# Optimization experiments

Measured on AMD Instinct MI355X. Metric: run time of the kernel, lower is better.

The kernel has to match this reference:

```python
import jax, jax.numpy as jnp
import numpy as np

B = 256      # events
N_SV = 64    # secondary vertices per event
N_TRK = 512  # tracks per event
N_PFC = 512  # PF candidates per event
K = 8        # kNN neighbors
H = 32       # hidden dim


def _lin_init(key, fan_in, fan_out):
    k1, k2 = jax.random.split(key)
    lim = 1.0 / np.sqrt(fan_in)
    W = jax.random.uniform(k1, (fan_in, fan_out), minval=-lim, maxval=lim, dtype=jnp.float32)
    b = jax.random.uniform(k2, (fan_out,), minval=-lim, maxval=lim, dtype=jnp.float32)
    return W, b


def setup_inputs() -> dict:
    key = jax.random.key(0)
    ks = jax.random.split(key, 16)
    inp = {
        'x_sv': jax.random.normal(ks[0], (B * N_SV, 14), dtype=jnp.float32),
        'x_trk': jax.random.normal(ks[1], (B * N_TRK, 30), dtype=jnp.float32),
        'x_pfc': jax.random.normal(ks[2], (B * N_PFC, 10), dtype=jnp.float32),
        'batch_sv': jnp.repeat(jnp.arange(B, dtype=jnp.int64), N_SV),
        'batch_trk': jnp.repeat(jnp.arange(B, dtype=jnp.int64), N_TRK),
        'batch_pfc': jnp.repeat(jnp.arange(B, dtype=jnp.int64), N_PFC),
    }
    inp['sv_W1'], inp['sv_b1'] = _lin_init(ks[3], 14, H)
    inp['sv_W2'], inp['sv_b2'] = _lin_init(ks[4], H, H)
    inp['trk_W1'], inp['trk_b1'] = _lin_init(ks[5], 30, H)
    inp['trk_W2'], inp['trk_b2'] = _lin_init(ks[6], H, H)
    inp['pfc_W1'], inp['pfc_b1'] = _lin_init(ks[7], 10, H)
    inp['pfc_W2'], inp['pfc_b2'] = _lin_init(ks[8], H, H)
    inp['conv_W'], inp['conv_b'] = _lin_init(ks[9], 2 * H, H)  # the single shared self.conv
    inp['out_W1'], inp['out_b1'] = _lin_init(ks[10], H, H)
    inp['out_W2'], inp['out_b2'] = _lin_init(ks[11], H, 1)
    return inp


def _encode(x, W1, b1, W2, b2):
    h = jax.nn.elu(x @ W1 + b1)
    return jax.nn.elu(h @ W2 + b2)


def _edge_conv(x_src, x_dst, W, b):
    # x_src [B,Ns,H] source set, x_dst [B,Nd,H] destination/query set.
    # kNN: for each dst node, K nearest src nodes (per event) by Euclidean dist.
    d2 = (jnp.sum(x_dst * x_dst, -1)[:, :, None]
          - 2.0 * jnp.einsum('bnd,bmd->bnm', x_dst, x_src)
          + jnp.sum(x_src * x_src, -1)[:, None, :])  # [B,Nd,Ns]
    _, idx = jax.lax.top_k(-d2, K)                     # [B,Nd,K]
    x_j = jax.vmap(lambda s, i: s[i])(x_src, idx)      # [B,Nd,K,H]
    x_i = jnp.broadcast_to(x_dst[:, :, None, :], x_j.shape)
    e = jnp.concatenate([x_i, x_j - x_i], axis=-1)     # [B,Nd,K,2H]
    m = jax.nn.elu(e @ W + b)                          # edge MLP
    return jnp.max(m, axis=2)                          # max aggregation [B,Nd,H]


def reference(x_sv, x_trk, x_pfc, batch_sv, batch_trk, batch_pfc,
              sv_W1, sv_b1, sv_W2, sv_b2,
              trk_W1, trk_b1, trk_W2, trk_b2,
              pfc_W1, pfc_b1, pfc_W2, pfc_b2,
              conv_W, conv_b, out_W1, out_b1, out_W2, out_b2):
    sv = _encode(x_sv, sv_W1, sv_b1, sv_W2, sv_b2).reshape(B, N_SV, H)
    trk = _encode(x_trk, trk_W1, trk_b1, trk_W2, trk_b2).reshape(B, N_TRK, H)
    pfc = _encode(x_pfc, pfc_W1, pfc_b1, pfc_W2, pfc_b2).reshape(B, N_PFC, H)

    feats1 = _edge_conv(sv, trk, conv_W, conv_b)     # sv -> trk
    feats2 = _edge_conv(pfc, trk, conv_W, conv_b)    # pfc -> trk
    feats3 = _edge_conv(feats1, feats2, conv_W, conv_b)  # feats1 -> feats2 (both trk-sized)

    # avg_pool_x(batch_trk, feats3, batch_trk): per-event mean
    f = feats3.reshape(B * N_TRK, H)
    s = jax.ops.segment_sum(f, batch_trk, num_segments=B)
    cnt = jax.ops.segment_sum(jnp.ones((B * N_TRK,), f.dtype), batch_trk, num_segments=B)
    pooled = s / cnt[:, None]

    out = jax.nn.sigmoid(jax.nn.elu(pooled @ out_W1 + out_b1) @ out_W2 + out_b2)  # [B,1]
    return out, jnp.arange(B, dtype=jnp.int64)
```

## Files before the change

### kernel.cpp

```cpp
#include <hip/hip_runtime.h>
#include <math.h>

#define NB 256
#define KNN 8

typedef __attribute__((ext_vector_type(8))) short short8;
typedef __attribute__((ext_vector_type(4))) float f32x4;

__device__ __forceinline__ float elu_f(float x) {
    return x > 0.f ? x : __expf(x) - 1.f;
}

__device__ __forceinline__ unsigned bf16rn(float x) {
    unsigned u = __float_as_uint(x);
    return (u + 0x7FFFu + ((u >> 16) & 1u)) >> 16;
}

__device__ __forceinline__ void bfsplit(float x, short& h, short& l) {
    unsigned hu = bf16rn(x);
    h = (short)hu;
    l = (short)bf16rn(x - __uint_as_float(hu << 16));
}

__device__ __forceinline__ void cex(unsigned& a, unsigned& b) {
    unsigned lo = min(a, b), hi = max(a, b);
    a = lo; b = hi;
}

__device__ __forceinline__ void sort8(unsigned* s) {
    cex(s[0], s[1]); cex(s[2], s[3]); cex(s[4], s[5]); cex(s[6], s[7]);
    cex(s[0], s[2]); cex(s[1], s[3]); cex(s[4], s[6]); cex(s[5], s[7]);
    cex(s[1], s[2]); cex(s[5], s[6]);
    cex(s[0], s[4]); cex(s[1], s[5]); cex(s[2], s[6]); cex(s[3], s[7]);
    cex(s[2], s[4]); cex(s[3], s[5]);
    cex(s[1], s[2]); cex(s[3], s[4]); cex(s[5], s[6]);
}

__device__ __forceinline__ void merge8(unsigned* v, const unsigned* s) {
#pragma unroll
    for (int i = 0; i < 8; i++) v[i] = min(v[i], s[7 - i]);
    cex(v[0], v[4]); cex(v[1], v[5]); cex(v[2], v[6]); cex(v[3], v[7]);
    cex(v[0], v[2]); cex(v[1], v[3]); cex(v[4], v[6]); cex(v[5], v[7]);
    cex(v[0], v[1]); cex(v[2], v[3]); cex(v[4], v[5]); cex(v[6], v[7]);
}

template<int FIN, int MODE>
__device__ void encode_mfma_body(const float* __restrict__ x,
    const float* __restrict__ W1, const float* __restrict__ b1,
    const float* __restrict__ W2, const float* __restrict__ b2,
    const float* __restrict__ conv_W, const float* __restrict__ conv_b,
    float* __restrict__ enc, float* __restrict__ e1,
    unsigned short* __restrict__ hiP, unsigned short* __restrict__ loP,
    float* __restrict__ nrmP,
    int blk, float* __restrict__ sx)
{
    int tid = threadIdx.x;
    int lane = tid & 63, wv = tid >> 6;
    int c = lane & 15, kg = lane >> 4;
    size_t node0 = (size_t)blk * 256;

    {
        const float* xb = x + node0 * FIN;
        for (int i = tid; i < 8192; i += 256) {
            int n = i >> 5, f = i & 31;
            sx[i] = (f < FIN) ? xb[n * FIN + f] : 0.f;
        }
    }
    __syncthreads();

    int rb = wv * 64;

#pragma unroll
    for (int ph = 0; ph < 3; ph++) {
        short8 Bh0, Bl0, Bh1, Bl1;
#pragma unroll
        for (int e = 0; e < 8; e++) {
            int kk = kg * 8 + e;
            float w0, w1;
            if (ph == 0) {
                w0 = (kk < FIN) ? W1[kk * 32 + c] : 0.f;
                w1 = (kk < FIN) ? W1[kk * 32 + 16 + c] : 0.f;
            } else if (ph == 1) {
                w0 = W2[kk * 32 + c];
                w1 = W2[kk * 32 + 16 + c];
            } else {
                w0 = conv_W[1024 + kk * 32 + c];
                w1 = conv_W[1024 + kk * 32 + 16 + c];
                if (MODE == 1) {
                    w0 = conv_W[kk * 32 + c] - w0;
                    w1 = conv_W[kk * 32 + 16 + c] - w1;
                }
            }
            short h, l;
            bfsplit(w0, h, l); Bh0[e] = h; Bl0[e] = l;
            bfsplit(w1, h, l); Bh1[e] = h; Bl1[e] = l;
        }
        float bias0, bias1;
        if (ph == 0)      { bias0 = b1[c]; bias1 = b1[16 + c]; }
        else if (ph == 1) { bias0 = b2[c]; bias1 = b2[16 + c]; }
        else              { bias0 = (MODE == 1) ? conv_b[c] : 0.f;
                            bias1 = (MODE == 1) ? conv_b[16 + c] : 0.f; }

#pragma unroll
        for (int t = 0; t < 4; t++) {
            int tb = rb + t * 16;
            int arow = tb + c;
            const float* ap = sx + arow * 32 + kg * 8;
            float4 a0 = *(const float4*)(ap);
            float4 a1 = *(const float4*)(ap + 4);
            float av[8] = {a0.x, a0.y, a0.z, a0.w, a1.x, a1.y, a1.z, a1.w};
            short8 Ah, Al;
#pragma unroll
            for (int e = 0; e < 8; e++) {
                short h, l;
                bfsplit(av[e], h, l);
                Ah[e] = h; Al[e] = l;
            }

            if (MODE == 0 && ph == 2) {
                float nr = 0.f;
#pragma unroll
                for (int e = 0; e < 8; e++) nr = fmaf(av[e], av[e], nr);
                nr += __shfl_xor(nr, 16);
                nr += __shfl_xor(nr, 32);
                if (kg == 0) nrmP[node0 + arow] = nr;
                *(short8*)(hiP + (node0 + arow) * 32 + kg * 8) = Ah;
                *(short8*)(loP + (node0 + arow) * 32 + kg * 8) = Al;
            }

            f32x4 acc0 = {bias0, bias0, bias0, bias0};
            f32x4 acc1 = {bias1, bias1, bias1, bias1};
            acc0 = __builtin_amdgcn_mfma_f32_16x16x32_bf16(Al, Bh0, acc0, 0, 0, 0);
            acc0 = __builtin_amdgcn_mfma_f32_16x16x32_bf16(Ah, Bl0, acc0, 0, 0, 0);
            acc0 = __builtin_amdgcn_mfma_f32_16x16x32_bf16(Ah, Bh0, acc0, 0, 0, 0);
            acc1 = __builtin_amdgcn_mfma_f32_16x16x32_bf16(Al, Bh1, acc1, 0, 0, 0);
            acc1 = __builtin_amdgcn_mfma_f32_16x16x32_bf16(Ah, Bl1, acc1, 0, 0, 0);
            acc1 = __builtin_amdgcn_mfma_f32_16x16x32_bf16(Ah, Bh1, acc1, 0, 0, 0);

            int drow = tb + kg * 4;
            if (ph < 2) {
#pragma unroll
                for (int r = 0; r < 4; r++) {
                    float v0 = elu_f(acc0[r]);
                    float v1 = elu_f(acc1[r]);
                    sx[(drow + r) * 32 + c] = v0;
                    sx[(drow + r) * 32 + 16 + c] = v1;
                    if (MODE == 1 && ph == 1) {
                        size_t off = (node0 + drow + r) * 32 + c;
                        enc[off] = v0;
                        enc[off + 16] = v1;
                    }
                }
            } else {
#pragma unroll
                for (int r = 0; r < 4; r++) {
                    size_t off = (node0 + drow + r) * 32 + c;
                    e1[off] = acc0[r];
                    e1[off + 16] = acc1[r];
                }
            }
        }
    }
}

__global__ __launch_bounds__(256) void encode_all_kernel(
    const float* __restrict__ x_sv, const float* __restrict__ x_trk, const float* __restrict__ x_pfc,
    const float* __restrict__ sv_W1, const float* __restrict__ sv_b1,
    const float* __restrict__ sv_W2, const float* __restrict__ sv_b2,
    const float* __restrict__ trk_W1, const float* __restrict__ trk_b1,
    const float* __restrict__ trk_W2, const float* __restrict__ trk_b2,
    const float* __restrict__ pfc_W1, const float* __restrict__ pfc_b1,
    const float* __restrict__ pfc_W2, const float* __restrict__ pfc_b2,
    const float* __restrict__ conv_W, const float* __restrict__ conv_b,
    float* __restrict__ trk_enc,
    float* __restrict__ Y1, float* __restrict__ Y2,
    float* __restrict__ f1base,
    unsigned short* __restrict__ svHi, unsigned short* __restrict__ svLo, float* __restrict__ nrm_sv,
    unsigned short* __restrict__ pfcHi, unsigned short* __restrict__ pfcLo, float* __restrict__ nrm_pfc)
{
    __shared__ float sx[8192];
    int bid = blockIdx.x;
    if (bid < 64)
        encode_mfma_body<14, 0>(x_sv, sv_W1, sv_b1, sv_W2, sv_b2, conv_W, conv_b,
                                nullptr, Y1, svHi, svLo, nrm_sv, bid, sx);
    else if (bid < 576)
        encode_mfma_body<30, 1>(x_trk, trk_W1, trk_b1, trk_W2, trk_b2, conv_W, conv_b,
                                trk_enc, f1base, nullptr, nullptr, nullptr, bid - 64, sx);
    else
        encode_mfma_body<10, 0>(x_pfc, pfc_W1, pfc_b1, pfc_W2, pfc_b2, conv_W, conv_b,
                                nullptr, Y2, pfcHi, pfcLo, nrm_pfc, bid - 576, sx);
}

__device__ __forceinline__ void knn_build_B(const float* __restrict__ dstF,
                                            int dstbase, int c, int kg,
                                            short8& Bh, short8& Bl, float& nd)
{
    const float* brow = dstF + (size_t)(dstbase + c) * 32 + kg * 8;
    float4 b0 = *(const float4*)(brow);
    float4 b1 = *(const float4*)(brow + 4);
    float bx[8] = {b0.x, b0.y, b0.z, b0.w, b1.x, b1.y, b1.z, b1.w};
    nd = 0.f;
#pragma unroll
    for (int i = 0; i < 8; i++) {
        float xv = bx[i];
        nd = fmaf(xv, xv, nd);
        short h, l;
        bfsplit(xv, h, l);
        Bh[i] = h; Bl[i] = l;
    }
    nd += __shfl_xor(nd, 16);
    nd += __shfl_xor(nd, 32);
}

template<int NT>
__device__ __forceinline__ void knn_scan(
    const unsigned short* __restrict__ srcHi, const unsigned short* __restrict__ srcLo,
    const float* __restrict__ snrm,
    short8 Bh, short8 Bl, float nd, int c, int kg,
    unsigned* key)
{
    for (int t = 0; t < NT; t += 2) {
        unsigned cand[8];
#pragma unroll
        for (int u = 0; u < 2; u++) {
            int tt = t + u;
            size_t arow = ((size_t)(tt * 16 + c)) * 32 + (size_t)kg * 8;
            short8 Ah = *(const short8*)(srcHi + arow);
            short8 Al = *(const short8*)(srcLo + arow);
            f32x4 acc = {0.f, 0.f, 0.f, 0.f};
            acc = __builtin_amdgcn_mfma_f32_16x16x32_bf16(Al, Bl, acc, 0, 0, 0);
            acc = __builtin_amdgcn_mfma_f32_16x16x32_bf16(Al, Bh, acc, 0, 0, 0);
            acc = __builtin_amdgcn_mfma_f32_16x16x32_bf16(Ah, Bl, acc, 0, 0, 0);
            acc = __builtin_amdgcn_mfma_f32_16x16x32_bf16(Ah, Bh, acc, 0, 0, 0);
            float4 sn = *(const float4*)(snrm + tt * 16 + kg * 4);
            int sb = tt * 16 + kg * 4;
            cand[u*4+0] = (__float_as_uint(fmaf(-2.f, acc[0], sn.x + nd)) & 0xFFFFFE00u) | (unsigned)(sb + 0);
            cand[u*4+1] = (__float_as_uint(fmaf(-2.f, acc[1], sn.y + nd)) & 0xFFFFFE00u) | (unsigned)(sb + 1);
            cand[u*4+2] = (__float_as_uint(fmaf(-2.f, acc[2], sn.z + nd)) & 0xFFFFFE00u) | (unsigned)(sb + 2);
            cand[u*4+3] = (__float_as_uint(fmaf(-2.f, acc[3], sn.w + nd)) & 0xFFFFFE00u) | (unsigned)(sb + 3);
        }
        sort8(cand);
        merge8(key, cand);
    }
}

__device__ __forceinline__ void knn_merge_lanes(unsigned* key)
{
    unsigned oth[8];
#pragma unroll
    for (int k = 0; k < 8; k++) oth[k] = __shfl_xor(key[k], 16);
    merge8(key, oth);
#pragma unroll
    for (int k = 0; k < 8; k++) oth[k] = __shfl_xor(key[k], 32);
    merge8(key, oth);
}

__device__ __forceinline__ void gather_max8(const float* __restrict__ Yb,
                                            const unsigned* key, int kg, float* m)
{
    const float* r0 = Yb + (size_t)(key[0] & 511u) * 32 + kg * 8;
    float4 a = *(const float4*)(r0);
    float4 b = *(const float4*)(r0 + 4);
    m[0] = a.x; m[1] = a.y; m[2] = a.z; m[3] = a.w;
    m[4] = b.x; m[5] = b.y; m[6] = b.z; m[7] = b.w;
#pragma unroll
    for (int k = 1; k < 8; k++) {
        const float* rr = Yb + (size_t)(key[k] & 511u) * 32 + kg * 8;
        float4 va = *(const float4*)(rr);
        float4 vb = *(const float4*)(rr + 4);
        m[0] = fmaxf(m[0], va.x); m[1] = fmaxf(m[1], va.y);
        m[2] = fmaxf(m[2], va.z); m[3] = fmaxf(m[3], va.w);
        m[4] = fmaxf(m[4], vb.x); m[5] = fmaxf(m[5], vb.y);
        m[6] = fmaxf(m[6], vb.z); m[7] = fmaxf(m[7], vb.w);
    }
}

__global__ __launch_bounds__(256) void knn12_kernel(
    const unsigned short* __restrict__ svHi, const unsigned short* __restrict__ svLo,
    const float* __restrict__ nrm_sv,
    const unsigned short* __restrict__ pfcHi, const unsigned short* __restrict__ pfcLo,
    const float* __restrict__ nrm_pfc,
    const float* __restrict__ trk_enc,
    const float* __restrict__ Y1, const float* __restrict__ Y2,
    const float* __restrict__ f1base, float* __restrict__ f2,
    unsigned short* __restrict__ f1Hi, unsigned short* __restrict__ f1Lo,
    float* __restrict__ nrm_f1,
    float* __restrict__ Y3, float* __restrict__ B3,
    const float* __restrict__ conv_W, const float* __restrict__ conv_b)
{
    int bid = blockIdx.x;
    int e = bid & 255, j = bid >> 8;
    int tid = threadIdx.x;
    int lane = tid & 63, wave = tid >> 6;
    int c = lane & 15, kg = lane >> 4;
    int dstbase = j * 64 + wave * 16;
    size_t trow = (size_t)e * 512 + dstbase + c;

    short8 WYh0, WYl0, WYh1, WYl1, WDh0, WDl0, WDh1, WDl1;
#pragma unroll
    for (int ee = 0; ee < 8; ee++) {
        int kk = kg * 8 + ee;
        float y0 = conv_W[1024 + kk * 32 + c];
        float y1 = conv_W[1024 + kk * 32 + 16 + c];
        float d0 = conv_W[kk * 32 + c] - y0;
        float d1 = conv_W[kk * 32 + 16 + c] - y1;
        short h, l;
        bfsplit(y0, h, l); WYh0[ee] = h; WYl0[ee] = l;
        bfsplit(y1, h, l); WYh1[ee] = h; WYl1[ee] = l;
        bfsplit(d0, h, l); WDh0[ee] = h; WDl0[ee] = l;
        bfsplit(d1, h, l); WDh1[ee] = h; WDl1[ee] = l;
    }
    float bd0 = conv_b[c], bd1 = conv_b[16 + c];

    short8 Bh, Bl;
    float nd;
    knn_build_B(trk_enc + (size_t)e * 512 * 32, dstbase, c, kg, Bh, Bl, nd);

    unsigned key2[8];
#pragma unroll
    for (int k = 0; k < 8; k++) key2[k] = 0xFFFFFFFFu;
    knn_scan<32>(pfcHi + (size_t)e * 512 * 32, pfcLo + (size_t)e * 512 * 32,
                 nrm_pfc + e * 512, Bh, Bl, nd, c, kg, key2);
    knn_merge_lanes(key2);

    unsigned key1[8];
#pragma unroll
    for (int k = 0; k < 8; k++) key1[k] = 0xFFFFFFFFu;
    knn_scan<4>(svHi + (size_t)e * 64 * 32, svLo + (size_t)e * 64 * 32,
                nrm_sv + e * 64, Bh, Bl, nd, c, kg, key1);
    knn_merge_lanes(key1);

    const float* bp = f1base + trow * 32 + kg * 8;
    float4 bb0 = *(const float4*)(bp);
    float4 bb1 = *(const float4*)(bp + 4);
    float base[8] = {bb0.x, bb0.y, bb0.z, bb0.w, bb1.x, bb1.y, bb1.z, bb1.w};

    float m[8];
    gather_max8(Y2 + (size_t)e * 512 * 32, key2, kg, m);
    float v2[8];
    short8 Fh, Fl;
#pragma unroll
    for (int i = 0; i < 8; i++) {
        v2[i] = elu_f(base[i] + m[i]);
        short h, l;
        bfsplit(v2[i], h, l);
        Fh[i] = h; Fl[i] = l;
    }
    {
        float4* op = (float4*)(f2 + trow * 32 + kg * 8);
        op[0] = (float4){v2[0], v2[1], v2[2], v2[3]};
        op[1] = (float4){v2[4], v2[5], v2[6], v2[7]};
    }

    gather_max8(Y1 + (size_t)e * 64 * 32, key1, kg, m);
    float v1[8];
    float nr = 0.f;
    short8 Hh, Hl;
#pragma unroll
    for (int i = 0; i < 8; i++) {
        v1[i] = elu_f(base[i] + m[i]);
        nr = fmaf(v1[i], v1[i], nr);
        short h, l;
        bfsplit(v1[i], h, l);
        Hh[i] = h; Hl[i] = l;
    }
    nr += __shfl_xor(nr, 16);
    nr += __shfl_xor(nr, 32);
    if (kg == 0) nrm_f1[trow] = nr;
    *(short8*)(f1Hi + trow * 32 + kg * 8) = Hh;
    *(short8*)(f1Lo + trow * 32 + kg * 8) = Hl;

    f32x4 a0 = {0.f, 0.f, 0.f, 0.f}, a1 = {0.f, 0.f, 0.f, 0.f};
    a0 = __builtin_amdgcn_mfma_f32_16x16x32_bf16(Hl, WYh0, a0, 0, 0, 0);
    a0 = __builtin_amdgcn_mfma_f32_16x16x32_bf16(Hh, WYl0, a0, 0, 0, 0);
    a0 = __builtin_amdgcn_mfma_f32_16x16x32_bf16(Hh, WYh0, a0, 0, 0, 0);
    a1 = __builtin_amdgcn_mfma_f32_16x16x32_bf16(Hl, WYh1, a1, 0, 0, 0);
    a1 = __builtin_amdgcn_mfma_f32_16x16x32_bf16(Hh, WYl1, a1, 0, 0, 0);
    a1 = __builtin_amdgcn_mfma_f32_16x16x32_bf16(Hh, WYh1, a1, 0, 0, 0);
    f32x4 q0 = {bd0, bd0, bd0, bd0}, q1 = {bd1, bd1, bd1, bd1};
    q0 = __builtin_amdgcn_mfma_f32_16x16x32_bf16(Fl, WDh0, q0, 0, 0, 0);
    q0 = __builtin_amdgcn_mfma_f32_16x16x32_bf16(Fh, WDl0, q0, 0, 0, 0);
    q0 = __builtin_amdgcn_mfma_f32_16x16x32_bf16(Fh, WDh0, q0, 0, 0, 0);
    q1 = __builtin_amdgcn_mfma_f32_16x16x32_bf16(Fl, WDh1, q1, 0, 0, 0);
    q1 = __builtin_amdgcn_mfma_f32_16x16x32_bf16(Fh, WDl1, q1, 0, 0, 0);
    q1 = __builtin_amdgcn_mfma_f32_16x16x32_bf16(Fh, WDh1, q1, 0, 0, 0);

    int drow = dstbase + kg * 4;
#pragma unroll
    for (int r = 0; r < 4; r++) {
        size_t off = ((size_t)e * 512 + drow + r) * 32 + c;
        Y3[off] = a0[r];  Y3[off + 16] = a1[r];
        B3[off] = q0[r];  B3[off + 16] = q1[r];
    }
}

__global__ __launch_bounds__(256) void knn3_kernel(
    const unsigned short* __restrict__ f1Hi, const unsigned short* __restrict__ f1Lo,
    const float* __restrict__ nrm_f1,
    const float* __restrict__ f2,
    const float* __restrict__ Y3, const float* __restrict__ B3,
    float* __restrict__ pool)
{
    __shared__ float sp[4][32];
    int bid = blockIdx.x;
    int e = bid & 255, j = bid >> 8;
    int tid = threadIdx.x;
    int lane = tid & 63, wave = tid >> 6;
    int c = lane & 15, kg = lane >> 4;
    int dstbase = j * 64 + wave * 16;
    size_t trow = (size_t)e * 512 + dstbase + c;

    short8 Bh, Bl;
    float nd;
    knn_build_B(f2 + (size_t)e * 512 * 32, dstbase, c, kg, Bh, Bl, nd);

    unsigned key[8];
#pragma unroll
    for (int k = 0; k < 8; k++) key[k] = 0xFFFFFFFFu;
    knn_scan<32>(f1Hi + (size_t)e * 512 * 32, f1Lo + (size_t)e * 512 * 32,
                 nrm_f1 + e * 512, Bh, Bl, nd, c, kg, key);
    knn_merge_lanes(key);

    float m[8];
    gather_max8(Y3 + (size_t)e * 512 * 32, key, kg, m);

    const float* bp = B3 + trow * 32 + kg * 8;
    float4 bb0 = *(const float4*)(bp);
    float4 bb1 = *(const float4*)(bp + 4);
    float base[8] = {bb0.x, bb0.y, bb0.z, bb0.w, bb1.x, bb1.y, bb1.z, bb1.w};

    float r[8];
#pragma unroll
    for (int i = 0; i < 8; i++) r[i] = elu_f(base[i] + m[i]);

#pragma unroll
    for (int off = 1; off < 16; off <<= 1) {
#pragma unroll
        for (int i = 0; i < 8; i++) r[i] += __shfl_xor(r[i], off);
    }
    if (c == 0) {
#pragma unroll
        for (int i = 0; i < 8; i++) sp[wave][kg * 8 + i] = r[i];
    }
    __syncthreads();
    if (tid < 32)
        pool[((size_t)e * 8 + j) * 32 + tid] =
            sp[0][tid] + sp[1][tid] + sp[2][tid] + sp[3][tid];
}

__global__ __launch_bounds__(64) void final_kernel(
    const float* __restrict__ pool,
    const float* __restrict__ W1, const float* __restrict__ b1,
    const float* __restrict__ W2, const float* __restrict__ b2,
    float* __restrict__ outp)
{
    int b = blockIdx.x;
    int lane = threadIdx.x, c = lane & 31;
    __shared__ float sp[32];
    __shared__ float sh1[32];
    if (lane < 32) {
        float s = 0.f;
#pragma unroll
        for (int jj = 0; jj < 8; jj++)
            s += pool[((size_t)b * 8 + jj) * 32 + c];
        sp[c] = s * (1.0f / 512.0f);
    }
    __syncthreads();
    if (lane < 32) {
        float h = b1[c];
#pragma unroll
        for (int d = 0; d < 32; d++) h = fmaf(sp[d], W1[d * 32 + c], h);
        sh1[c] = elu_f(h);
    }
    __syncthreads();
    if (lane == 0) {
        float o = b2[0];
#pragma unroll
        for (int d = 0; d < 32; d++) o = fmaf(sh1[d], W2[d], o);
        o = 1.f / (1.f + __expf(-o));
        outp[b] = o;
        outp[NB + b] = (float)b;
    }
}

extern "C" void kernel_launch(void* const* d_in, const int* in_sizes, int n_in,
                              void* d_out, int out_size, void* d_ws, size_t ws_size,
                              hipStream_t stream) {
    const float* x_sv  = (const float*)d_in[0];
    const float* x_trk = (const float*)d_in[1];
    const float* x_pfc = (const float*)d_in[2];
    const float* sv_W1  = (const float*)d_in[6];
    const float* sv_b1  = (const float*)d_in[7];
    const float* sv_W2  = (const float*)d_in[8];
    const float* sv_b2  = (const float*)d_in[9];
    const float* trk_W1 = (const float*)d_in[10];
    const float* trk_b1 = (const float*)d_in[11];
    const float* trk_W2 = (const float*)d_in[12];
    const float* trk_b2 = (const float*)d_in[13];
    const float* pfc_W1 = (const float*)d_in[14];
    const float* pfc_b1 = (const float*)d_in[15];
    const float* pfc_W2 = (const float*)d_in[16];
    const float* pfc_b2 = (const float*)d_in[17];
    const float* conv_W = (const float*)d_in[18];
    const float* conv_b = (const float*)d_in[19];
    const float* out_W1 = (const float*)d_in[20];
    const float* out_b1 = (const float*)d_in[21];
    const float* out_W2 = (const float*)d_in[22];
    const float* out_b2 = (const float*)d_in[23];

    float* ws = (float*)d_ws;
    const size_t SV_E  = (size_t)NB * 64 * 32;
    const size_t TRK_E = (size_t)NB * 512 * 32;
    float* f1base  = ws;
    float* f2      = f1base + TRK_E;
    float* trk_enc = f2 + TRK_E;
    float* Y1      = trk_enc + TRK_E;
    float* Y2      = Y1 + SV_E;
    unsigned short* svHi  = (unsigned short*)(Y2 + TRK_E);
    unsigned short* svLo  = svHi + SV_E;
    unsigned short* pfcHi = svLo + SV_E;
    unsigned short* pfcLo = pfcHi + TRK_E;
    unsigned short* f1Hi  = pfcLo + TRK_E;
    unsigned short* f1Lo  = f1Hi + TRK_E;
    float* nrm_sv  = (float*)(f1Lo + TRK_E);
    float* nrm_pfc = nrm_sv + (size_t)NB * 64;
    float* nrm_f1  = nrm_pfc + (size_t)NB * 512;
    float* Y3   = trk_enc;
    float* B3   = f1base;
    float* pool = (float*)svHi;

    encode_all_kernel<<<1088, 256, 0, stream>>>(
        x_sv, x_trk, x_pfc,
        sv_W1, sv_b1, sv_W2, sv_b2,
        trk_W1, trk_b1, trk_W2, trk_b2,
        pfc_W1, pfc_b1, pfc_W2, pfc_b2,
        conv_W, conv_b,
        trk_enc, Y1, Y2, f1base,
        svHi, svLo, nrm_sv, pfcHi, pfcLo, nrm_pfc);

    knn12_kernel<<<2048, 256, 0, stream>>>(svHi, svLo, nrm_sv,
                                           pfcHi, pfcLo, nrm_pfc,
                                           trk_enc, Y1, Y2,
                                           f1base, f2, f1Hi, f1Lo, nrm_f1,
                                           Y3, B3, conv_W, conv_b);

    knn3_kernel<<<2048, 256, 0, stream>>>(f1Hi, f1Lo, nrm_f1, f2, Y3, B3, pool);

    final_kernel<<<NB, 64, 0, stream>>>(pool, out_W1, out_b1, out_W2, out_b2, (float*)d_out);
}
```

Baseline: 295.8 us.

## Interleave two independent kNN scan streams and fuse final MLP via last-block atomic

The 512-candidate kNN scan is split into two interleaved halves with separate top-8 key lists, merged at the end. This breaks the serial dependency chain of sort/merge so MFMA and merge work from the two halves can overlap. Separately, the final per-event MLP kernel is removed. Its work is done inside knn3 by whichever block of each event arrives last, detected with an atomic counter that knn12 resets, which saves one launch. This adds register pressure, threadfence overhead, and a workspace counter that relies on stream ordering for its reset.

```diff
diff --git a/kernel.cpp b/kernel.cpp
--- a/kernel.cpp
+++ b/kernel.cpp
@@ -212,6 +212,32 @@
     nd += __shfl_xor(nd, 32);
 }
 
+__device__ __forceinline__ void knn_batch(
+    const unsigned short* __restrict__ srcHi, const unsigned short* __restrict__ srcLo,
+    const float* __restrict__ snrm,
+    short8 Bh, short8 Bl, float nd, int c, int kg, int t0,
+    unsigned* cand)
+{
+#pragma unroll
+    for (int u = 0; u < 2; u++) {
+        int tt = t0 + u;
+        size_t arow = ((size_t)(tt * 16 + c)) * 32 + (size_t)kg * 8;
+        short8 Ah = *(const short8*)(srcHi + arow);
+        short8 Al = *(const short8*)(srcLo + arow);
+        f32x4 acc = {0.f, 0.f, 0.f, 0.f};
+        acc = __builtin_amdgcn_mfma_f32_16x16x32_bf16(Al, Bl, acc, 0, 0, 0);
+        acc = __builtin_amdgcn_mfma_f32_16x16x32_bf16(Al, Bh, acc, 0, 0, 0);
+        acc = __builtin_amdgcn_mfma_f32_16x16x32_bf16(Ah, Bl, acc, 0, 0, 0);
+        acc = __builtin_amdgcn_mfma_f32_16x16x32_bf16(Ah, Bh, acc, 0, 0, 0);
+        float4 sn = *(const float4*)(snrm + tt * 16 + kg * 4);
+        int sb = tt * 16 + kg * 4;
+        cand[u*4+0] = (__float_as_uint(fmaf(-2.f, acc[0], sn.x + nd)) & 0xFFFFFE00u) | (unsigned)(sb + 0);
+        cand[u*4+1] = (__float_as_uint(fmaf(-2.f, acc[1], sn.y + nd)) & 0xFFFFFE00u) | (unsigned)(sb + 1);
+        cand[u*4+2] = (__float_as_uint(fmaf(-2.f, acc[2], sn.z + nd)) & 0xFFFFFE00u) | (unsigned)(sb + 2);
+        cand[u*4+3] = (__float_as_uint(fmaf(-2.f, acc[3], sn.w + nd)) & 0xFFFFFE00u) | (unsigned)(sb + 3);
+    }
+}
+
 template<int NT>
 __device__ __forceinline__ void knn_scan(
     const unsigned short* __restrict__ srcHi, const unsigned short* __restrict__ srcLo,
@@ -221,27 +247,29 @@
 {
     for (int t = 0; t < NT; t += 2) {
         unsigned cand[8];
-#pragma unroll
-        for (int u = 0; u < 2; u++) {
-            int tt = t + u;
-            size_t arow = ((size_t)(tt * 16 + c)) * 32 + (size_t)kg * 8;
-            short8 Ah = *(const short8*)(srcHi + arow);
-            short8 Al = *(const short8*)(srcLo + arow);
-            f32x4 acc = {0.f, 0.f, 0.f, 0.f};
-            acc = __builtin_amdgcn_mfma_f32_16x16x32_bf16(Al, Bl, acc, 0, 0, 0);
-            acc = __builtin_amdgcn_mfma_f32_16x16x32_bf16(Al, Bh, acc, 0, 0, 0);
-            acc = __builtin_amdgcn_mfma_f32_16x16x32_bf16(Ah, Bl, acc, 0, 0, 0);
-            acc = __builtin_amdgcn_mfma_f32_16x16x32_bf16(Ah, Bh, acc, 0, 0, 0);
-            float4 sn = *(const float4*)(snrm + tt * 16 + kg * 4);
-            int sb = tt * 16 + kg * 4;
-            cand[u*4+0] = (__float_as_uint(fmaf(-2.f, acc[0], sn.x + nd)) & 0xFFFFFE00u) | (unsigned)(sb + 0);
-            cand[u*4+1] = (__float_as_uint(fmaf(-2.f, acc[1], sn.y + nd)) & 0xFFFFFE00u) | (unsigned)(sb + 1);
-            cand[u*4+2] = (__float_as_uint(fmaf(-2.f, acc[2], sn.z + nd)) & 0xFFFFFE00u) | (unsigned)(sb + 2);
-            cand[u*4+3] = (__float_as_uint(fmaf(-2.f, acc[3], sn.w + nd)) & 0xFFFFFE00u) | (unsigned)(sb + 3);
-        }
+        knn_batch(srcHi, srcLo, snrm, Bh, Bl, nd, c, kg, t, cand);
         sort8(cand);
         merge8(key, cand);
     }
+}
+
+__device__ __forceinline__ void knn_scan32_dual(
+    const unsigned short* __restrict__ srcHi, const unsigned short* __restrict__ srcLo,
+    const float* __restrict__ snrm,
+    short8 Bh, short8 Bl, float nd, int c, int kg,
+    unsigned* key)
+{
+    unsigned keyB[8];
+#pragma unroll
+    for (int k = 0; k < 8; k++) keyB[k] = 0xFFFFFFFFu;
+    for (int t = 0; t < 16; t += 2) {
+        unsigned ca[8], cb[8];
+        knn_batch(srcHi, srcLo, snrm, Bh, Bl, nd, c, kg, t, ca);
+        knn_batch(srcHi, srcLo, snrm, Bh, Bl, nd, c, kg, 16 + t, cb);
+        sort8(ca); merge8(key, ca);
+        sort8(cb); merge8(keyB, cb);
+    }
+    merge8(key, keyB);
 }
 
 __device__ __forceinline__ void knn_merge_lanes(unsigned* key)
@@ -286,7 +314,8 @@
     unsigned short* __restrict__ f1Hi, unsigned short* __restrict__ f1Lo,
     float* __restrict__ nrm_f1,
     float* __restrict__ Y3, float* __restrict__ B3,
-    const float* __restrict__ conv_W, const float* __restrict__ conv_b)
+    const float* __restrict__ conv_W, const float* __restrict__ conv_b,
+    int* __restrict__ cnt)
 {
     int bid = blockIdx.x;
     int e = bid & 255, j = bid >> 8;
@@ -295,6 +324,8 @@
     int c = lane & 15, kg = lane >> 4;
     int dstbase = j * 64 + wave * 16;
     size_t trow = (size_t)e * 512 + dstbase + c;
+
+    if (j == 0 && tid == 0) cnt[e] = 0;
 
     short8 WYh0, WYl0, WYh1, WYl1, WDh0, WDl0, WDh1, WDl1;
 #pragma unroll
@@ -319,8 +350,8 @@
     unsigned key2[8];
 #pragma unroll
     for (int k = 0; k < 8; k++) key2[k] = 0xFFFFFFFFu;
-    knn_scan<32>(pfcHi + (size_t)e * 512 * 32, pfcLo + (size_t)e * 512 * 32,
-                 nrm_pfc + e * 512, Bh, Bl, nd, c, kg, key2);
+    knn_scan32_dual(pfcHi + (size_t)e * 512 * 32, pfcLo + (size_t)e * 512 * 32,
+                    nrm_pfc + e * 512, Bh, Bl, nd, c, kg, key2);
     knn_merge_lanes(key2);
 
     unsigned key1[8];
@@ -399,9 +430,15 @@
     const float* __restrict__ nrm_f1,
     const float* __restrict__ f2,
     const float* __restrict__ Y3, const float* __restrict__ B3,
-    float* __restrict__ pool)
+    float* __restrict__ pool, int* __restrict__ cnt,
+    const float* __restrict__ out_W1, const float* __restrict__ out_b1,
+    const float* __restrict__ out_W2, const float* __restrict__ out_b2,
+    float* __restrict__ outp)
 {
     __shared__ float sp[4][32];
+    __shared__ float spf[32];
+    __shared__ float sh1[32];
+    __shared__ int sflag;
     int bid = blockIdx.x;
     int e = bid & 255, j = bid >> 8;
     int tid = threadIdx.x;
@@ -417,8 +454,8 @@
     unsigned key[8];
 #pragma unroll
     for (int k = 0; k < 8; k++) key[k] = 0xFFFFFFFFu;
-    knn_scan<32>(f1Hi + (size_t)e * 512 * 32, f1Lo + (size_t)e * 512 * 32,
-                 nrm_f1 + e * 512, Bh, Bl, nd, c, kg, key);
+    knn_scan32_dual(f1Hi + (size_t)e * 512 * 32, f1Lo + (size_t)e * 512 * 32,
+                    nrm_f1 + e * 512, Bh, Bl, nd, c, kg, key);
     knn_merge_lanes(key);
 
     float m[8];
@@ -446,40 +483,40 @@
     if (tid < 32)
         pool[((size_t)e * 8 + j) * 32 + tid] =
             sp[0][tid] + sp[1][tid] + sp[2][tid] + sp[3][tid];
-}
-
-__global__ __launch_bounds__(64) void final_kernel(
-    const float* __restrict__ pool,
-    const float* __restrict__ W1, const float* __restrict__ b1,
-    const float* __restrict__ W2, const float* __restrict__ b2,
-    float* __restrict__ outp)
-{
-    int b = blockIdx.x;
-    int lane = threadIdx.x, c = lane & 31;
-    __shared__ float sp[32];
-    __shared__ float sh1[32];
-    if (lane < 32) {
-        float s = 0.f;
-#pragma unroll
-        for (int jj = 0; jj < 8; jj++)
-            s += pool[((size_t)b * 8 + jj) * 32 + c];
-        sp[c] = s * (1.0f / 512.0f);
-    }
+
+    __threadfence();
     __syncthreads();
-    if (lane < 32) {
-        float h = b1[c];
-#pragma unroll
-        for (int d = 0; d < 32; d++) h = fmaf(sp[d], W1[d * 32 + c], h);
-        sh1[c] = elu_f(h);
+    if (tid == 0) {
+        int old = atomicAdd(&cnt[e], 1);
+        sflag = (old == 7);
     }
     __syncthreads();
-    if (lane == 0) {
-        float o = b2[0];
-#pragma unroll
-        for (int d = 0; d < 32; d++) o = fmaf(sh1[d], W2[d], o);
-        o = 1.f / (1.f + __expf(-o));
-        outp[b] = o;
-        outp[NB + b] = (float)b;
+    if (sflag) {
+        __threadfence();
+        if (tid < 32) {
+            float s = 0.f;
+#pragma unroll
+            for (int jj = 0; jj < 8; jj++)
+                s += pool[((size_t)e * 8 + jj) * 32 + tid];
+            spf[tid] = s * (1.0f / 512.0f);
+        }
+        __syncthreads();
+        if (tid < 32) {
+            float h = out_b1[tid];
+#pragma unroll
+            for (int d = 0; d < 32; d++)
+                h = fmaf(spf[d], out_W1[d * 32 + tid], h);
+            sh1[tid] = elu_f(h);
+        }
+        __syncthreads();
+        if (tid == 0) {
+            float o = out_b2[0];
+#pragma unroll
+            for (int d = 0; d < 32; d++) o = fmaf(sh1[d], out_W2[d], o);
+            o = 1.f / (1.f + __expf(-o));
+            outp[e] = o;
+            outp[NB + e] = (float)e;
+        }
     }
 }
 
@@ -525,6 +562,7 @@
     float* nrm_sv  = (float*)(f1Lo + TRK_E);
     float* nrm_pfc = nrm_sv + (size_t)NB * 64;
     float* nrm_f1  = nrm_pfc + (size_t)NB * 512;
+    int*   cnt     = (int*)(nrm_f1 + (size_t)NB * 512);
     float* Y3   = trk_enc;
     float* B3   = f1base;
     float* pool = (float*)svHi;
@@ -542,9 +580,10 @@
                                            pfcHi, pfcLo, nrm_pfc,
                                            trk_enc, Y1, Y2,
                                            f1base, f2, f1Hi, f1Lo, nrm_f1,
-                                           Y3, B3, conv_W, conv_b);
-
-    knn3_kernel<<<2048, 256, 0, stream>>>(f1Hi, f1Lo, nrm_f1, f2, Y3, B3, pool);
-
-    final_kernel<<<NB, 64, 0, stream>>>(pool, out_W1, out_b1, out_W2, out_b2, (float*)d_out);
-}
+                                           Y3, B3, conv_W, conv_b, cnt);
+
+    knn3_kernel<<<2048, 256, 0, stream>>>(f1Hi, f1Lo, nrm_f1, f2, Y3, B3,
+                                          pool, cnt,
+                                          out_W1, out_b1, out_W2, out_b2,
+                                          (float*)d_out);
+}
```

Result: slower. 477.7 us (+61.5%).
